# Kernel tuning notes

Measured on AMD Instinct MI355X. Metric: run time of the kernel, lower is better.

## Reference

```python
import jax, jax.numpy as jnp
import numpy as np

N_NODES = 50000
N_EDGES = 1600000
F_IN = 33
F_OUT = 128
HEADS = 2


def _add_self_loops(row, col, n):
    loop = jnp.arange(n, dtype=row.dtype)
    return jnp.concatenate([row, loop]), jnp.concatenate([col, loop])


def gcn_conv(x, row, col, w, W, b):
    # PyG GCNConv with edge_weight: add self-loops (weight 1), symmetric norm.
    n = x.shape[0]
    row, col = _add_self_loops(row, col, n)
    w = jnp.concatenate([w, jnp.ones((n,), x.dtype)])
    deg = jax.ops.segment_sum(w, col, num_segments=n)
    dinv = jnp.where(deg > 0, jax.lax.rsqrt(deg), 0.0)
    norm = dinv[row] * w * dinv[col]            # [E+N]
    xl = x @ W                                   # [N, F_OUT]
    out = jax.ops.segment_sum(norm[:, None] * xl[row], col, num_segments=n)
    return out + b


def gat_conv(x, row, col, W, att_src, att_dst, b):
    # PyG GATConv, heads=2, concat=False, eval-mode (no attention dropout).
    n = x.shape[0]
    row, col = _add_self_loops(row, col, n)
    xl = (x @ W).reshape(n, HEADS, F_OUT)        # [N, H, C]
    a_src = (xl * att_src).sum(-1)               # [N, H]
    a_dst = (xl * att_dst).sum(-1)               # [N, H]
    e = jax.nn.leaky_relu(a_src[row] + a_dst[col], 0.2)  # [E+N, H]
    m = jax.ops.segment_max(e, col, num_segments=n)      # per-dst max (stable)
    e = jnp.exp(e - m[col])
    s = jax.ops.segment_sum(e, col, num_segments=n)
    alpha = e / s[col]                           # edge softmax per dst node
    out = jax.ops.segment_sum(alpha[:, :, None] * xl[row], col, num_segments=n)
    return out.mean(axis=1) + b                  # concat=False -> head mean


def setup_inputs() -> dict:
    key = jax.random.key(0)
    ks = jax.random.split(key, 16)
    s_in = 1.0 / np.sqrt(F_IN)
    s_h = 1.0 / np.sqrt(F_OUT)
    inp = {
        "target_x": jax.random.normal(ks[0], (N_NODES, F_IN), jnp.float32),
        "target_edge_index": jax.random.randint(ks[1], (2, N_EDGES), 0, N_NODES, jnp.int32),
        "target_weight": jax.random.uniform(ks[2], (N_EDGES,), jnp.float32),
        "gcn_W": jax.random.normal(ks[3], (F_IN, F_OUT), jnp.float32) * s_in,
        "gcn_b": jnp.zeros((F_OUT,), jnp.float32),
        "gat1_W": jax.random.normal(ks[4], (F_OUT, HEADS * F_OUT), jnp.float32) * s_h,
        "gat1_as": jax.random.normal(ks[5], (HEADS, F_OUT), jnp.float32) * s_h,
        "gat1_ad": jax.random.normal(ks[6], (HEADS, F_OUT), jnp.float32) * s_h,
        "gat1_b": jnp.zeros((F_OUT,), jnp.float32),
        "gat2_W": jax.random.normal(ks[7], (F_OUT, HEADS * F_OUT), jnp.float32) * s_h,
        "gat2_as": jax.random.normal(ks[8], (HEADS, F_OUT), jnp.float32) * s_h,
        "gat2_ad": jax.random.normal(ks[9], (HEADS, F_OUT), jnp.float32) * s_h,
        "gat2_b": jnp.zeros((F_OUT,), jnp.float32),
        "fc1_W": jax.random.normal(ks[10], (F_OUT, F_OUT), jnp.float32) * s_h,
        "fc1_b": jnp.zeros((F_OUT,), jnp.float32),
        "fc2_W": jax.random.normal(ks[11], (F_OUT, F_OUT), jnp.float32) * s_h,
        "fc2_b": jnp.zeros((F_OUT,), jnp.float32),
        "pro_bias": jax.random.uniform(ks[12], (1, F_OUT), jnp.float32, -0.2, 0.2),
    }
    return inp


def _forward(target_x, target_weight, gcn_W, gcn_b, gat1_W, gat1_as, gat1_ad,
             gat1_b, gat2_W, gat2_as, gat2_ad, gat2_b, fc1_W, fc1_b,
             fc2_W, fc2_b, pro_bias, row, col):
    # layer 0: GCN + ReLU
    x = jax.nn.relu(gcn_conv(target_x, row, col, target_weight, gcn_W, gcn_b))
    # layer 1: GAT + ReLU, then sigmoid-gated blend
    xt = jax.nn.relu(gat_conv(x, row, col, gat1_W, gat1_as, gat1_ad, gat1_b))
    z = jax.nn.sigmoid(xt @ fc1_W + fc1_b + x @ fc2_W + fc2_b + pro_bias)
    x = z * xt + (1.0 - z) * x
    # layer 2: GAT (no ReLU on last layer), gated blend
    xt = gat_conv(x, row, col, gat2_W, gat2_as, gat2_ad, gat2_b)
    z = jax.nn.sigmoid(xt @ fc1_W + fc1_b + x @ fc2_W + fc2_b + pro_bias)
    return z * xt + (1.0 - z) * x


def reference(target_x, target_edge_index, target_weight, gcn_W, gcn_b,
              gat1_W, gat1_as, gat1_ad, gat1_b, gat2_W, gat2_as, gat2_ad,
              gat2_b, fc1_W, fc1_b, fc2_W, fc2_b, pro_bias):
    row, col = target_edge_index[0], target_edge_index[1]
    return _forward(target_x, target_weight, gcn_W, gcn_b, gat1_W, gat1_as,
                    gat1_ad, gat1_b, gat2_W, gat2_as, gat2_ad, gat2_b,
                    fc1_W, fc1_b, fc2_W, fc2_b, pro_bias, row, col)
```

## Files before the change

kernel.cpp:

```cpp
#include <hip/hip_runtime.h>

#define F_IN 33
#define FP 36
#define C 128
#define GROWS 16
#define MAXDEG 128

__device__ __forceinline__ unsigned short f2bf(float f) {
  unsigned u = __float_as_uint(f);
  unsigned r = (u + 0x7fff + ((u >> 16) & 1)) >> 16;
  return (unsigned short)r;
}
__device__ __forceinline__ unsigned pack2(float lo, float hi) {
  return (unsigned)f2bf(lo) | ((unsigned)f2bf(hi) << 16);
}
__device__ __forceinline__ float bflo(unsigned u) { return __uint_as_float(u << 16); }
__device__ __forceinline__ float bfhi(unsigned u) { return __uint_as_float(u & 0xffff0000u); }


__global__ void count_kernel(const int* __restrict__ col, const float* __restrict__ w,
                             int* __restrict__ cnt, float* __restrict__ deg, int E) {
  int e = blockIdx.x * blockDim.x + threadIdx.x;
  if (e < E) {
    int c = col[e];
    atomicAdd(&cnt[c], 1);
    atomicAdd(&deg[c], w[e]);
  }
}

__global__ void scan1_kernel(const int* __restrict__ cnt, int* __restrict__ out,
                             int* __restrict__ bsum, int n) {
  __shared__ int lds[256];
  int t = threadIdx.x;
  int base = blockIdx.x * 1024 + t * 4;
  int v0 = (base + 0 < n) ? cnt[base + 0] : 0;
  int v1 = (base + 1 < n) ? cnt[base + 1] : 0;
  int v2 = (base + 2 < n) ? cnt[base + 2] : 0;
  int v3 = (base + 3 < n) ? cnt[base + 3] : 0;
  int tot = v0 + v1 + v2 + v3;
  lds[t] = tot;
  __syncthreads();
  for (int o = 1; o < 256; o <<= 1) {
    int x = (t >= o) ? lds[t - o] : 0;
    __syncthreads();
    lds[t] += x;
    __syncthreads();
  }
  int excl = lds[t] - tot;
  if (t == 255) bsum[blockIdx.x] = lds[255];
  if (base + 0 < n) out[base + 0] = excl;
  if (base + 1 < n) out[base + 1] = excl + v0;
  if (base + 2 < n) out[base + 2] = excl + v0 + v1;
  if (base + 3 < n) out[base + 3] = excl + v0 + v1 + v2;
}

__global__ void scan2_kernel(int* __restrict__ bsum, int nb) {
  __shared__ int lds[256];
  int t = threadIdx.x;
  int v = (t < nb) ? bsum[t] : 0;
  lds[t] = v;
  __syncthreads();
  for (int o = 1; o < 256; o <<= 1) {
    int x = (t >= o) ? lds[t - o] : 0;
    __syncthreads();
    lds[t] += x;
    __syncthreads();
  }
  if (t < nb) bsum[t] = lds[t] - v;
}

__global__ void scan3_dinv_kernel(int* __restrict__ off, const int* __restrict__ bsum,
                                  const float* __restrict__ deg, float* __restrict__ dinv,
                                  int n, int N) {
  int i = blockIdx.x * blockDim.x + threadIdx.x;
  if (i < n) off[i] += bsum[i >> 10];
  if (i < N) dinv[i] = rsqrtf(deg[i] + 1.0f);
}

__global__ void scatter_kernel(const int* __restrict__ row, const int* __restrict__ col,
                               const float* __restrict__ w, const int* __restrict__ off,
                               const float* __restrict__ dinv, int* __restrict__ cur,
                               int2* __restrict__ sedge, int E) {
  int e = blockIdx.x * blockDim.x + threadIdx.x;
  if (e < E) {
    int c = col[e];
    int r = row[e];
    int p = off[c] + atomicAdd(&cur[c], 1);
    sedge[p] = make_int2(r, __float_as_int(dinv[r] * w[e]));
  }
}


__global__ void prep_dots_kernel(const float* __restrict__ W1, const float* __restrict__ as1,
                                 const float* __restrict__ ad1, const float* __restrict__ W2,
                                 const float* __restrict__ as2, const float* __restrict__ ad2,
                                 float* __restrict__ attv) {
  int t = blockIdx.x * 256 + threadIdx.x;
  if (t >= 1024) return;
  int layer = t >> 9, rem = t & 511, sd = rem >> 8, rem2 = rem & 255;
  int h = rem2 >> 7, k = rem2 & 127;
  const float* W = layer ? W2 : W1;
  const float* att = sd ? (layer ? ad2 : ad1) : (layer ? as2 : as1);
  float s = 0.f;
  for (int c2 = 0; c2 < C; c2++) s += W[k * 2 * C + h * C + c2] * att[h * C + c2];
  attv[t] = s;
}

__global__ void prep_repack_kernel(const float* __restrict__ W1, const float* __restrict__ W2,
                                   float* __restrict__ Wp1, float* __restrict__ Wp2) {
  int t = blockIdx.x * 256 + threadIdx.x;
  int layer = t >> 15, rem = t & 32767, hk = rem >> 7, j = rem & 127;
  int h = hk >> 7, k = hk & 127;
  const float* W = layer ? W2 : W1;
  float* Wp = layer ? Wp2 : Wp1;
  Wp[hk * C + j] = W[k * 2 * C + h * C + j];
}

__global__ void convert_x_kernel(const float* __restrict__ x, unsigned* __restrict__ X36U, int N) {
  int t = blockIdx.x * blockDim.x + threadIdx.x;
  if (t >= N * (FP / 2)) return;
  int n = t / (FP / 2);
  int p = t - n * (FP / 2);
  int c0 = 2 * p, c1 = 2 * p + 1;
  float f0 = (c0 < F_IN) ? x[n * F_IN + c0] : 0.f;
  float f1 = (c1 < F_IN) ? x[n * F_IN + c1] : 0.f;
  X36U[t] = pack2(f0, f1);
}


__global__ __launch_bounds__(256) void gcn_agg33_kernel(
    const unsigned* __restrict__ X36U, const int* __restrict__ off,
    const int2* __restrict__ sedge, const float* __restrict__ dinv,
    float* __restrict__ Xagg, int N) {
  int c = blockIdx.x * 4 + (threadIdx.x >> 6);
  if (c >= N) return;
  int l = threadIdx.x & 63;
  bool act = l < FP / 2;
  float dc = dinv[c];
  unsigned uc = act ? X36U[(unsigned)c * (FP / 2) + l] : 0u;
  float A0x = dc * bflo(uc), A0y = dc * bfhi(uc);
  float A1x = 0.f, A1y = 0.f, A2x = 0.f, A2y = 0.f, A3x = 0.f, A3y = 0.f;
  int p = off[c], p1 = off[c + 1];
  for (; p + 4 <= p1; p += 4) {
    int2 e0 = sedge[p + 0], e1 = sedge[p + 1], e2 = sedge[p + 2], e3 = sedge[p + 3];
    unsigned u0 = 0, u1 = 0, u2 = 0, u3 = 0;
    if (act) {
      u0 = X36U[(unsigned)e0.x * (FP / 2) + l];
      u1 = X36U[(unsigned)e1.x * (FP / 2) + l];
      u2 = X36U[(unsigned)e2.x * (FP / 2) + l];
      u3 = X36U[(unsigned)e3.x * (FP / 2) + l];
    }
    float w0 = __int_as_float(e0.y), w1 = __int_as_float(e1.y);
    float w2 = __int_as_float(e2.y), w3 = __int_as_float(e3.y);
    A0x += w0 * bflo(u0); A0y += w0 * bfhi(u0);
    A1x += w1 * bflo(u1); A1y += w1 * bfhi(u1);
    A2x += w2 * bflo(u2); A2y += w2 * bfhi(u2);
    A3x += w3 * bflo(u3); A3y += w3 * bfhi(u3);
  }
  for (; p < p1; p++) {
    int2 e0 = sedge[p];
    unsigned u0 = act ? X36U[(unsigned)e0.x * (FP / 2) + l] : 0u;
    float w0 = __int_as_float(e0.y);
    A0x += w0 * bflo(u0); A0y += w0 * bfhi(u0);
  }
  if (act) {
    float2 o;
    o.x = dc * (A0x + A1x + A2x + A3x);
    o.y = dc * (A0y + A1y + A2y + A3y);
    ((float2*)Xagg)[(unsigned)c * (FP / 2) + l] = o;
  }
}

__global__ void gemm36_kernel(const float* __restrict__ Xagg, const float* __restrict__ W,
                              const float* __restrict__ b, const float* __restrict__ ws,
                              const float* __restrict__ wd, float* __restrict__ H,
                              unsigned short* __restrict__ Hb, float* __restrict__ asrc,
                              float* __restrict__ adst, int N) {
  int n0 = blockIdx.x * GROWS;
  int j = threadIdx.x;
  __shared__ float xr[GROWS * FP];
  __shared__ float xls[GROWS * 132];
  {
    const float4* src = (const float4*)(Xagg + (size_t)n0 * FP);
    float4* dst = (float4*)xr;
    for (int i = j; i < GROWS * FP / 4; i += 128) dst[i] = src[i];
  }
  __syncthreads();
  float acc[GROWS];
  #pragma unroll
  for (int r = 0; r < GROWS; r++) acc[r] = 0.f;
  #pragma unroll 3
  for (int k = 0; k < F_IN; k++) {
    float wv = W[k * C + j];
    #pragma unroll
    for (int r = 0; r < GROWS; r++) acc[r] += xr[r * FP + k] * wv;
  }
  #pragma unroll
  for (int r = 0; r < GROWS; r++) {
    int n = n0 + r;
    float v = fmaxf(acc[r] + b[j], 0.f);
    if (n < N) {
      H[(size_t)n * C + j] = v;
      Hb[(size_t)n * C + j] = f2bf(v);
    }
    xls[r * 132 + j] = v;
  }
  __syncthreads();
  int r = j >> 3, sub = j & 7;
  float sa0 = 0.f, sd0 = 0.f, sa1 = 0.f, sd1 = 0.f;
  for (int k = sub; k < C; k += 8) {
    float v = xls[r * 132 + k];
    sa0 += v * ws[k];      sd0 += v * wd[k];
    sa1 += v * ws[C + k];  sd1 += v * wd[C + k];
  }
  #pragma unroll
  for (int o = 4; o > 0; o >>= 1) {
    sa0 += __shfl_down(sa0, o); sd0 += __shfl_down(sd0, o);
    sa1 += __shfl_down(sa1, o); sd1 += __shfl_down(sd1, o);
  }
  int n = n0 + r;
  if (sub == 0 && n < N) {
    asrc[n * 2 + 0] = sa0; adst[n * 2 + 0] = sd0;
    asrc[n * 2 + 1] = sa1; adst[n * 2 + 1] = sd1;
  }
}

__global__ __launch_bounds__(256) void gat_agg_kernel(
    const unsigned* __restrict__ HbU, const float* __restrict__ asrc,
    const float* __restrict__ adst, const int* __restrict__ off,
    const int2* __restrict__ sedge, unsigned* __restrict__ AggU, int N) {
  __shared__ float2 lsc[4][MAXDEG];
  int slot = threadIdx.x >> 6;
  int c = blockIdx.x * 4 + slot;
  if (c >= N) return;
  int l = threadIdx.x & 63;
  float2 adc = ((const float2*)adst)[c];
  float2 asc = ((const float2*)asrc)[c];
  int p0 = off[c], p1 = off[c + 1];
  int deg = p1 - p0;
  float e00 = asc.x + adc.x; e00 = e00 > 0.f ? e00 : 0.2f * e00;
  float e01 = asc.y + adc.y; e01 = e01 > 0.f ? e01 : 0.2f * e01;
  float m0 = e00, m1 = e01;
  for (int p = p0 + l; p < p1; p += 64) {
    int r = sedge[p].x;
    float2 av = ((const float2*)asrc)[r];
    float e0 = av.x + adc.x; e0 = e0 > 0.f ? e0 : 0.2f * e0;
    float e1 = av.y + adc.y; e1 = e1 > 0.f ? e1 : 0.2f * e1;
    int i = p - p0;
    if (i < MAXDEG) lsc[slot][i] = make_float2(e0, e1);
    m0 = fmaxf(m0, e0); m1 = fmaxf(m1, e1);
  }
  #pragma unroll
  for (int o = 32; o > 0; o >>= 1) {
    m0 = fmaxf(m0, __shfl_xor(m0, o));
    m1 = fmaxf(m1, __shfl_xor(m1, o));
  }
  int nl = deg < MAXDEG ? deg : MAXDEG;
  float s0 = 0.f, s1 = 0.f;
  for (int i = l; i < nl; i += 64) {
    float2 sc = lsc[slot][i];
    float a0 = __expf(sc.x - m0), a1 = __expf(sc.y - m1);
    lsc[slot][i] = make_float2(a0, a1);
    s0 += a0; s1 += a1;
  }
  for (int p = p0 + MAXDEG + l; p < p1; p += 64) {
    int r = sedge[p].x;
    float2 av = ((const float2*)asrc)[r];
    float e0 = av.x + adc.x; e0 = e0 > 0.f ? e0 : 0.2f * e0;
    float e1 = av.y + adc.y; e1 = e1 > 0.f ? e1 : 0.2f * e1;
    s0 += __expf(e0 - m0); s1 += __expf(e1 - m1);
  }
  #pragma unroll
  for (int o = 32; o > 0; o >>= 1) { s0 += __shfl_xor(s0, o); s1 += __shfl_xor(s1, o); }
  float w0 = __expf(e00 - m0), w1 = __expf(e01 - m1);
  s0 += w0; s1 += w1;
  float inv0 = 1.f / s0, inv1 = 1.f / s1;
  unsigned uc = HbU[(unsigned)c * 64 + l];
  float a00 = w0 * bflo(uc), a01 = w0 * bfhi(uc);
  float a10 = w1 * bflo(uc), a11 = w1 * bfhi(uc);
  float b00 = 0.f, b01 = 0.f, b10 = 0.f, b11 = 0.f;
  int i = 0;
  for (; i + 8 <= nl; i += 8) {
    int r0 = sedge[p0 + i + 0].x, r1 = sedge[p0 + i + 1].x;
    int r2 = sedge[p0 + i + 2].x, r3 = sedge[p0 + i + 3].x;
    int r4 = sedge[p0 + i + 4].x, r5 = sedge[p0 + i + 5].x;
    int r6 = sedge[p0 + i + 6].x, r7 = sedge[p0 + i + 7].x;
    unsigned u0 = HbU[(unsigned)r0 * 64 + l];
    unsigned u1 = HbU[(unsigned)r1 * 64 + l];
    unsigned u2 = HbU[(unsigned)r2 * 64 + l];
    unsigned u3 = HbU[(unsigned)r3 * 64 + l];
    unsigned u4 = HbU[(unsigned)r4 * 64 + l];
    unsigned u5 = HbU[(unsigned)r5 * 64 + l];
    unsigned u6 = HbU[(unsigned)r6 * 64 + l];
    unsigned u7 = HbU[(unsigned)r7 * 64 + l];
    float2 f0 = lsc[slot][i + 0], f1 = lsc[slot][i + 1];
    float2 f2 = lsc[slot][i + 2], f3 = lsc[slot][i + 3];
    float2 f4 = lsc[slot][i + 4], f5 = lsc[slot][i + 5];
    float2 f6 = lsc[slot][i + 6], f7 = lsc[slot][i + 7];
    a00 += f0.x * bflo(u0); a01 += f0.x * bfhi(u0); a10 += f0.y * bflo(u0); a11 += f0.y * bfhi(u0);
    b00 += f1.x * bflo(u1); b01 += f1.x * bfhi(u1); b10 += f1.y * bflo(u1); b11 += f1.y * bfhi(u1);
    a00 += f2.x * bflo(u2); a01 += f2.x * bfhi(u2); a10 += f2.y * bflo(u2); a11 += f2.y * bfhi(u2);
    b00 += f3.x * bflo(u3); b01 += f3.x * bfhi(u3); b10 += f3.y * bflo(u3); b11 += f3.y * bfhi(u3);
    a00 += f4.x * bflo(u4); a01 += f4.x * bfhi(u4); a10 += f4.y * bflo(u4); a11 += f4.y * bfhi(u4);
    b00 += f5.x * bflo(u5); b01 += f5.x * bfhi(u5); b10 += f5.y * bflo(u5); b11 += f5.y * bfhi(u5);
    a00 += f6.x * bflo(u6); a01 += f6.x * bfhi(u6); a10 += f6.y * bflo(u6); a11 += f6.y * bfhi(u6);
    b00 += f7.x * bflo(u7); b01 += f7.x * bfhi(u7); b10 += f7.y * bflo(u7); b11 += f7.y * bfhi(u7);
  }
  for (; i < nl; i++) {
    int r0 = sedge[p0 + i].x;
    unsigned u0 = HbU[(unsigned)r0 * 64 + l];
    float2 f0 = lsc[slot][i];
    a00 += f0.x * bflo(u0); a01 += f0.x * bfhi(u0);
    a10 += f0.y * bflo(u0); a11 += f0.y * bfhi(u0);
  }
  for (int p = p0 + MAXDEG; p < p1; p++) {
    int r = sedge[p].x;
    float2 av = ((const float2*)asrc)[r];
    float e0 = av.x + adc.x; e0 = e0 > 0.f ? e0 : 0.2f * e0;
    float e1 = av.y + adc.y; e1 = e1 > 0.f ? e1 : 0.2f * e1;
    float al0 = __expf(e0 - m0), al1 = __expf(e1 - m1);
    unsigned u0 = HbU[(unsigned)r * 64 + l];
    a00 += al0 * bflo(u0); a01 += al0 * bfhi(u0);
    a10 += al1 * bflo(u0); a11 += al1 * bfhi(u0);
  }
  AggU[(unsigned)c * 128 + l]      = pack2((a00 + b00) * inv0, (a01 + b01) * inv0);
  AggU[(unsigned)c * 128 + 64 + l] = pack2((a10 + b10) * inv1, (a11 + b11) * inv1);
}

__global__ void post_gemm_kernel(const unsigned* __restrict__ AggU, const float* __restrict__ Wp,
                                 const float* __restrict__ b, float* __restrict__ out,
                                 int relu, int N) {
  int n0 = blockIdx.x * GROWS;
  int j = threadIdx.x;
  __shared__ float als[GROWS * 260];
  {
    const uint2* src = (const uint2*)(AggU + (size_t)n0 * 128);
    for (int t = j; t < GROWS * 64; t += 128) {
      int row = t >> 6, cp = t & 63;
      uint2 u = (n0 + row < N) ? src[t] : make_uint2(0u, 0u);
      float* d = &als[row * 260 + cp * 4];
      d[0] = bflo(u.x); d[1] = bfhi(u.x); d[2] = bflo(u.y); d[3] = bfhi(u.y);
    }
  }
  __syncthreads();
  float acc[GROWS];
  #pragma unroll
  for (int r = 0; r < GROWS; r++) acc[r] = 0.f;
  #pragma unroll 2
  for (int k4 = 0; k4 < 256; k4 += 4) {
    float w0 = Wp[(k4 + 0) * C + j], w1 = Wp[(k4 + 1) * C + j];
    float w2 = Wp[(k4 + 2) * C + j], w3 = Wp[(k4 + 3) * C + j];
    #pragma unroll
    for (int r = 0; r < GROWS; r++) {
      float4 a = *(const float4*)&als[r * 260 + k4];
      acc[r] += a.x * w0 + a.y * w1 + a.z * w2 + a.w * w3;
    }
  }
  #pragma unroll
  for (int r = 0; r < GROWS; r++) {
    int n = n0 + r;
    if (n < N) {
      float v = 0.5f * acc[r] + b[j];
      if (relu) v = fmaxf(v, 0.f);
      out[(size_t)n * C + j] = v;
    }
  }
}

__global__ void blend_kernel(const float* __restrict__ xt, const float* __restrict__ x,
                             const float* __restrict__ fc1W, const float* __restrict__ fc1b,
                             const float* __restrict__ fc2W, const float* __restrict__ fc2b,
                             const float* __restrict__ pb, float* __restrict__ out,
                             unsigned short* __restrict__ Hb2, const float* __restrict__ ws,
                             const float* __restrict__ wd, float* __restrict__ asrc,
                             float* __restrict__ adst, int dots, int N) {
  int n0 = blockIdx.x * GROWS;
  int j = threadIdx.x;
  __shared__ float xtr[GROWS * C];
  __shared__ float xr[GROWS * C];
  __shared__ float xls[GROWS * 132];
  {
    float4* a4 = (float4*)xtr;
    float4* b4 = (float4*)xr;
    const float4* xt4 = (const float4*)xt;
    const float4* x4 = (const float4*)x;
    for (int i = j; i < GROWS * C / 4; i += 128) {
      int n = n0 + (i * 4) / C;
      if (n < N) {
        a4[i] = xt4[n0 * (C / 4) + i];
        b4[i] = x4[n0 * (C / 4) + i];
      } else {
        a4[i] = make_float4(0.f, 0.f, 0.f, 0.f);
        b4[i] = make_float4(0.f, 0.f, 0.f, 0.f);
      }
    }
  }
  __syncthreads();
  float s1[GROWS], s2[GROWS];
  #pragma unroll
  for (int r = 0; r < GROWS; r++) { s1[r] = 0.f; s2[r] = 0.f; }
  #pragma unroll 2
  for (int k4 = 0; k4 < C; k4 += 4) {
    float w1a = fc1W[(k4 + 0) * C + j], w2a = fc2W[(k4 + 0) * C + j];
    float w1b = fc1W[(k4 + 1) * C + j], w2b = fc2W[(k4 + 1) * C + j];
    float w1c = fc1W[(k4 + 2) * C + j], w2c = fc2W[(k4 + 2) * C + j];
    float w1d = fc1W[(k4 + 3) * C + j], w2d = fc2W[(k4 + 3) * C + j];
    #pragma unroll
    for (int r = 0; r < GROWS; r++) {
      float4 t4 = *(const float4*)&xtr[r * C + k4];
      float4 x4 = *(const float4*)&xr[r * C + k4];
      s1[r] += t4.x * w1a + t4.y * w1b + t4.z * w1c + t4.w * w1d;
      s2[r] += x4.x * w2a + x4.y * w2b + x4.z * w2c + x4.w * w2d;
    }
  }
  float bb = fc1b[j] + fc2b[j] + pb[j];
  #pragma unroll
  for (int r = 0; r < GROWS; r++) {
    int n = n0 + r;
    float t = s1[r] + s2[r] + bb;
    float z = 1.f / (1.f + __expf(-t));
    float o = z * xtr[r * C + j] + (1.f - z) * xr[r * C + j];
    if (n < N) {
      out[(size_t)n * C + j] = o;
      if (dots) Hb2[(size_t)n * C + j] = f2bf(o);
    }
    xls[r * 132 + j] = o;
  }
  if (!dots) return;
  __syncthreads();
  int r = j >> 3, sub = j & 7;
  float sa0 = 0.f, sd0 = 0.f, sa1 = 0.f, sd1 = 0.f;
  for (int k = sub; k < C; k += 8) {
    float v = xls[r * 132 + k];
    sa0 += v * ws[k];      sd0 += v * wd[k];
    sa1 += v * ws[C + k];  sd1 += v * wd[C + k];
  }
  #pragma unroll
  for (int o = 4; o > 0; o >>= 1) {
    sa0 += __shfl_down(sa0, o); sd0 += __shfl_down(sd0, o);
    sa1 += __shfl_down(sa1, o); sd1 += __shfl_down(sd1, o);
  }
  int n = n0 + r;
  if (sub == 0 && n < N) {
    asrc[n * 2 + 0] = sa0; adst[n * 2 + 0] = sd0;
    asrc[n * 2 + 1] = sa1; adst[n * 2 + 1] = sd1;
  }
}


extern "C" void kernel_launch(void* const* d_in, const int* in_sizes, int n_in,
                              void* d_out, int out_size, void* d_ws, size_t ws_size,
                              hipStream_t stream) {
  const float* x_in  = (const float*)d_in[0];
  const int*   ei    = (const int*)d_in[1];
  const float* ew    = (const float*)d_in[2];
  const float* gcn_W = (const float*)d_in[3];
  const float* gcn_b = (const float*)d_in[4];
  const float* g1_W  = (const float*)d_in[5];
  const float* g1_as = (const float*)d_in[6];
  const float* g1_ad = (const float*)d_in[7];
  const float* g1_b  = (const float*)d_in[8];
  const float* g2_W  = (const float*)d_in[9];
  const float* g2_as = (const float*)d_in[10];
  const float* g2_ad = (const float*)d_in[11];
  const float* g2_b  = (const float*)d_in[12];
  const float* fc1_W = (const float*)d_in[13];
  const float* fc1_b = (const float*)d_in[14];
  const float* fc2_W = (const float*)d_in[15];
  const float* fc2_b = (const float*)d_in[16];
  const float* pb    = (const float*)d_in[17];

  const int N = in_sizes[0] / F_IN;
  const int E = in_sizes[2];
  const int* row = ei;
  const int* col = ei + E;

  char* ws = (char*)d_ws;
  size_t o = 0;
  auto alloc = [&](size_t bytes) -> void* {
    void* p = ws + o;
    o += (bytes + 255) & ~(size_t)255;
    return p;
  };
  int*   cnt   = (int*)alloc((size_t)(N + 1) * 4);
  int*   cur   = (int*)alloc((size_t)N * 4);
  float* deg   = (float*)alloc((size_t)N * 4);
  size_t zero_bytes = o;
  int*   off   = (int*)alloc((size_t)(N + 1) * 4);
  float* dinv  = (float*)alloc((size_t)N * 4);
  int*   bsum  = (int*)alloc(256 * 4);
  int2*  sedge = (int2*)alloc((size_t)E * 8);
  float* attv  = (float*)alloc(1024 * 4);
  float* Wp1   = (float*)alloc((size_t)256 * C * 4);
  float* Wp2   = (float*)alloc((size_t)256 * C * 4);
  float* asrc  = (float*)alloc((size_t)N * 2 * 4);
  float* adst  = (float*)alloc((size_t)N * 2 * 4);
  unsigned* X36U = (unsigned*)alloc((size_t)N * (FP / 2) * 4);
  float* Xagg  = (float*)alloc((size_t)N * FP * 4);
  float* H     = (float*)alloc((size_t)N * C * 4);
  unsigned short* Hb  = (unsigned short*)alloc((size_t)N * C * 2);
  unsigned* AggU = (unsigned*)alloc((size_t)N * 128 * 4);
  float* XT    = (float*)alloc((size_t)N * C * 4);
  float* H2    = (float*)alloc((size_t)N * C * 4);
  unsigned short* Hb2 = (unsigned short*)alloc((size_t)N * C * 2);
  (void)ws_size; (void)n_in; (void)out_size;

  float* ws1 = attv + 0,   *wd1 = attv + 256;
  float* ws2 = attv + 512, *wd2 = attv + 768;

  hipMemsetAsync(d_ws, 0, zero_bytes, stream);

  const int tb = 256;
  const int nP = N + 1;
  const int nb = (nP + 1023) / 1024;

  prep_dots_kernel<<<4, 256, 0, stream>>>(g1_W, g1_as, g1_ad, g2_W, g2_as, g2_ad, attv);
  prep_repack_kernel<<<256, 256, 0, stream>>>(g1_W, g2_W, Wp1, Wp2);
  convert_x_kernel<<<(N * (FP / 2) + tb - 1) / tb, tb, 0, stream>>>(x_in, X36U, N);

  count_kernel<<<(E + tb - 1) / tb, tb, 0, stream>>>(col, ew, cnt, deg, E);
  scan1_kernel<<<nb, 256, 0, stream>>>(cnt, off, bsum, nP);
  scan2_kernel<<<1, 256, 0, stream>>>(bsum, nb);
  scan3_dinv_kernel<<<(nP + tb - 1) / tb, tb, 0, stream>>>(off, bsum, deg, dinv, nP, N);
  scatter_kernel<<<(E + tb - 1) / tb, tb, 0, stream>>>(row, col, ew, off, dinv, cur, sedge, E);

  gcn_agg33_kernel<<<(N + 3) / 4, 256, 0, stream>>>(X36U, off, sedge, dinv, Xagg, N);
  gemm36_kernel<<<(N + GROWS - 1) / GROWS, C, 0, stream>>>(Xagg, gcn_W, gcn_b, ws1, wd1,
                                                           H, Hb, asrc, adst, N);

  gat_agg_kernel<<<(N + 3) / 4, 256, 0, stream>>>((const unsigned*)Hb, asrc, adst, off, sedge, AggU, N);
  post_gemm_kernel<<<(N + GROWS - 1) / GROWS, C, 0, stream>>>(AggU, Wp1, g1_b, XT, 1, N);
  blend_kernel<<<(N + GROWS - 1) / GROWS, C, 0, stream>>>(XT, H, fc1_W, fc1_b, fc2_W, fc2_b, pb,
                                                          H2, Hb2, ws2, wd2, asrc, adst, 1, N);

  gat_agg_kernel<<<(N + 3) / 4, 256, 0, stream>>>((const unsigned*)Hb2, asrc, adst, off, sedge, AggU, N);
  post_gemm_kernel<<<(N + GROWS - 1) / GROWS, C, 0, stream>>>(AggU, Wp2, g2_b, XT, 0, N);
  blend_kernel<<<(N + GROWS - 1) / GROWS, C, 0, stream>>>(XT, H2, fc1_W, fc1_b, fc2_W, fc2_b, pb,
                                                          (float*)d_out, (unsigned short*)0,
                                                          ws2, wd2, asrc, adst, 0, N);
}
```

Measured before the change: 1.007 ms.

## Drop LDS staging in dense GEMM kernels and store GAT aggregates in fp32

The gemm36, post_gemm and blend kernels no longer copy their input rows into shared memory behind a barrier. Each thread now reads the row data directly from global memory as broadcast float4 loads, with a separate scalar path for the partial last tile. The GAT aggregation output changes from packed bf16 to fp32, so post_gemm skips the unpack step, at the cost of twice the intermediate memory traffic. Dropping LDS staging frees shared memory and may raise occupancy, but it relies on the cache to serve the repeated per-thread reads of the same addresses.

```diff
diff --git a/kernel.cpp b/kernel.cpp
--- a/kernel.cpp
+++ b/kernel.cpp
@@ -171,29 +171,37 @@
   }
 }
 
-__global__ void gemm36_kernel(const float* __restrict__ Xagg, const float* __restrict__ W,
-                              const float* __restrict__ b, const float* __restrict__ ws,
-                              const float* __restrict__ wd, float* __restrict__ H,
-                              unsigned short* __restrict__ Hb, float* __restrict__ asrc,
-                              float* __restrict__ adst, int N) {
+__global__ __launch_bounds__(128) void gemm36_kernel(
+    const float* __restrict__ Xagg, const float* __restrict__ W,
+    const float* __restrict__ b, const float* __restrict__ wsv,
+    const float* __restrict__ wdv, float* __restrict__ H,
+    unsigned short* __restrict__ Hb, float* __restrict__ asrc,
+    float* __restrict__ adst, int N) {
   int n0 = blockIdx.x * GROWS;
   int j = threadIdx.x;
-  __shared__ float xr[GROWS * FP];
   __shared__ float xls[GROWS * 132];
-  {
-    const float4* src = (const float4*)(Xagg + (size_t)n0 * FP);
-    float4* dst = (float4*)xr;
-    for (int i = j; i < GROWS * FP / 4; i += 128) dst[i] = src[i];
-  }
-  __syncthreads();
   float acc[GROWS];
   #pragma unroll
   for (int r = 0; r < GROWS; r++) acc[r] = 0.f;
-  #pragma unroll 3
-  for (int k = 0; k < F_IN; k++) {
-    float wv = W[k * C + j];
+  if (n0 + GROWS <= N) {
+    for (int k4 = 0; k4 < 32; k4 += 4) {
+      float w0 = W[(k4 + 0) * C + j], w1 = W[(k4 + 1) * C + j];
+      float w2 = W[(k4 + 2) * C + j], w3 = W[(k4 + 3) * C + j];
+      #pragma unroll
+      for (int r = 0; r < GROWS; r++) {
+        float4 a = *(const float4*)(Xagg + (size_t)(n0 + r) * FP + k4);
+        acc[r] += a.x * w0 + a.y * w1 + a.z * w2 + a.w * w3;
+      }
+    }
+    float w32 = W[32 * C + j];
     #pragma unroll
-    for (int r = 0; r < GROWS; r++) acc[r] += xr[r * FP + k] * wv;
+    for (int r = 0; r < GROWS; r++) acc[r] += Xagg[(size_t)(n0 + r) * FP + 32] * w32;
+  } else {
+    int nr = N - n0;
+    for (int k = 0; k < F_IN; k++) {
+      float wv = W[k * C + j];
+      for (int r = 0; r < nr; r++) acc[r] += Xagg[(size_t)(n0 + r) * FP + k] * wv;
+    }
   }
   #pragma unroll
   for (int r = 0; r < GROWS; r++) {
@@ -210,8 +218,8 @@
   float sa0 = 0.f, sd0 = 0.f, sa1 = 0.f, sd1 = 0.f;
   for (int k = sub; k < C; k += 8) {
     float v = xls[r * 132 + k];
-    sa0 += v * ws[k];      sd0 += v * wd[k];
-    sa1 += v * ws[C + k];  sd1 += v * wd[C + k];
+    sa0 += v * wsv[k];      sd0 += v * wdv[k];
+    sa1 += v * wsv[C + k];  sd1 += v * wdv[C + k];
   }
   #pragma unroll
   for (int o = 4; o > 0; o >>= 1) {
@@ -228,7 +236,7 @@
 __global__ __launch_bounds__(256) void gat_agg_kernel(
     const unsigned* __restrict__ HbU, const float* __restrict__ asrc,
     const float* __restrict__ adst, const int* __restrict__ off,
-    const int2* __restrict__ sedge, unsigned* __restrict__ AggU, int N) {
+    const int2* __restrict__ sedge, float* __restrict__ Agg, int N) {
   __shared__ float2 lsc[4][MAXDEG];
   int slot = threadIdx.x >> 6;
   int c = blockIdx.x * 4 + slot;
@@ -323,37 +331,33 @@
     a00 += al0 * bflo(u0); a01 += al0 * bfhi(u0);
     a10 += al1 * bflo(u0); a11 += al1 * bfhi(u0);
   }
-  AggU[(unsigned)c * 128 + l]      = pack2((a00 + b00) * inv0, (a01 + b01) * inv0);
-  AggU[(unsigned)c * 128 + 64 + l] = pack2((a10 + b10) * inv1, (a11 + b11) * inv1);
-}
-
-__global__ void post_gemm_kernel(const unsigned* __restrict__ AggU, const float* __restrict__ Wp,
-                                 const float* __restrict__ b, float* __restrict__ out,
-                                 int relu, int N) {
+  ((float2*)Agg)[(size_t)c * 128 + l]      = make_float2((a00 + b00) * inv0, (a01 + b01) * inv0);
+  ((float2*)Agg)[(size_t)c * 128 + 64 + l] = make_float2((a10 + b10) * inv1, (a11 + b11) * inv1);
+}
+
+__global__ __launch_bounds__(128) void post_gemm_kernel(
+    const float* __restrict__ Agg, const float* __restrict__ Wp,
+    const float* __restrict__ b, float* __restrict__ out, int relu, int N) {
   int n0 = blockIdx.x * GROWS;
   int j = threadIdx.x;
-  __shared__ float als[GROWS * 260];
-  {
-    const uint2* src = (const uint2*)(AggU + (size_t)n0 * 128);
-    for (int t = j; t < GROWS * 64; t += 128) {
-      int row = t >> 6, cp = t & 63;
-      uint2 u = (n0 + row < N) ? src[t] : make_uint2(0u, 0u);
-      float* d = &als[row * 260 + cp * 4];
-      d[0] = bflo(u.x); d[1] = bfhi(u.x); d[2] = bflo(u.y); d[3] = bfhi(u.y);
-    }
-  }
-  __syncthreads();
   float acc[GROWS];
   #pragma unroll
   for (int r = 0; r < GROWS; r++) acc[r] = 0.f;
-  #pragma unroll 2
-  for (int k4 = 0; k4 < 256; k4 += 4) {
-    float w0 = Wp[(k4 + 0) * C + j], w1 = Wp[(k4 + 1) * C + j];
-    float w2 = Wp[(k4 + 2) * C + j], w3 = Wp[(k4 + 3) * C + j];
-    #pragma unroll
-    for (int r = 0; r < GROWS; r++) {
-      float4 a = *(const float4*)&als[r * 260 + k4];
-      acc[r] += a.x * w0 + a.y * w1 + a.z * w2 + a.w * w3;
+  if (n0 + GROWS <= N) {
+    for (int k4 = 0; k4 < 256; k4 += 4) {
+      float w0 = Wp[(k4 + 0) * C + j], w1 = Wp[(k4 + 1) * C + j];
+      float w2 = Wp[(k4 + 2) * C + j], w3 = Wp[(k4 + 3) * C + j];
+      #pragma unroll
+      for (int r = 0; r < GROWS; r++) {
+        float4 a = *(const float4*)(Agg + (size_t)(n0 + r) * 256 + k4);
+        acc[r] += a.x * w0 + a.y * w1 + a.z * w2 + a.w * w3;
+      }
+    }
+  } else {
+    int nr = N - n0;
+    for (int k = 0; k < 256; k++) {
+      float wv = Wp[k * C + j];
+      for (int r = 0; r < nr; r++) acc[r] += Agg[(size_t)(n0 + r) * 256 + k] * wv;
     }
   }
   #pragma unroll
@@ -367,64 +371,60 @@
   }
 }
 
-__global__ void blend_kernel(const float* __restrict__ xt, const float* __restrict__ x,
-                             const float* __restrict__ fc1W, const float* __restrict__ fc1b,
-                             const float* __restrict__ fc2W, const float* __restrict__ fc2b,
-                             const float* __restrict__ pb, float* __restrict__ out,
-                             unsigned short* __restrict__ Hb2, const float* __restrict__ ws,
-                             const float* __restrict__ wd, float* __restrict__ asrc,
-                             float* __restrict__ adst, int dots, int N) {
+__global__ __launch_bounds__(128) void blend_kernel(
+    const float* __restrict__ xt, const float* __restrict__ x,
+    const float* __restrict__ fc1W, const float* __restrict__ fc1b,
+    const float* __restrict__ fc2W, const float* __restrict__ fc2b,
+    const float* __restrict__ pb, float* __restrict__ out,
+    unsigned short* __restrict__ Hb2, const float* __restrict__ wsv,
+    const float* __restrict__ wdv, float* __restrict__ asrc,
+    float* __restrict__ adst, int dots, int N) {
   int n0 = blockIdx.x * GROWS;
   int j = threadIdx.x;
-  __shared__ float xtr[GROWS * C];
-  __shared__ float xr[GROWS * C];
   __shared__ float xls[GROWS * 132];
-  {
-    float4* a4 = (float4*)xtr;
-    float4* b4 = (float4*)xr;
-    const float4* xt4 = (const float4*)xt;
-    const float4* x4 = (const float4*)x;
-    for (int i = j; i < GROWS * C / 4; i += 128) {
-      int n = n0 + (i * 4) / C;
-      if (n < N) {
-        a4[i] = xt4[n0 * (C / 4) + i];
-        b4[i] = x4[n0 * (C / 4) + i];
-      } else {
-        a4[i] = make_float4(0.f, 0.f, 0.f, 0.f);
-        b4[i] = make_float4(0.f, 0.f, 0.f, 0.f);
+  float s1[GROWS], s2[GROWS];
+  #pragma unroll
+  for (int r = 0; r < GROWS; r++) { s1[r] = 0.f; s2[r] = 0.f; }
+  if (n0 + GROWS <= N) {
+    for (int k4 = 0; k4 < C; k4 += 4) {
+      float w1a = fc1W[(k4 + 0) * C + j], w2a = fc2W[(k4 + 0) * C + j];
+      float w1b = fc1W[(k4 + 1) * C + j], w2b = fc2W[(k4 + 1) * C + j];
+      float w1c = fc1W[(k4 + 2) * C + j], w2c = fc2W[(k4 + 2) * C + j];
+      float w1d = fc1W[(k4 + 3) * C + j], w2d = fc2W[(k4 + 3) * C + j];
+      #pragma unroll
+      for (int r = 0; r < GROWS; r++) {
+        float4 t4 = *(const float4*)(xt + (size_t)(n0 + r) * C + k4);
+        float4 x4 = *(const float4*)(x + (size_t)(n0 + r) * C + k4);
+        s1[r] += t4.x * w1a + t4.y * w1b + t4.z * w1c + t4.w * w1d;
+        s2[r] += x4.x * w2a + x4.y * w2b + x4.z * w2c + x4.w * w2d;
       }
     }
-  }
-  __syncthreads();
-  float s1[GROWS], s2[GROWS];
-  #pragma unroll
-  for (int r = 0; r < GROWS; r++) { s1[r] = 0.f; s2[r] = 0.f; }
-  #pragma unroll 2
-  for (int k4 = 0; k4 < C; k4 += 4) {
-    float w1a = fc1W[(k4 + 0) * C + j], w2a = fc2W[(k4 + 0) * C + j];
-    float w1b = fc1W[(k4 + 1) * C + j], w2b = fc2W[(k4 + 1) * C + j];
-    float w1c = fc1W[(k4 + 2) * C + j], w2c = fc2W[(k4 + 2) * C + j];
-    float w1d = fc1W[(k4 + 3) * C + j], w2d = fc2W[(k4 + 3) * C + j];
-    #pragma unroll
-    for (int r = 0; r < GROWS; r++) {
-      float4 t4 = *(const float4*)&xtr[r * C + k4];
-      float4 x4 = *(const float4*)&xr[r * C + k4];
-      s1[r] += t4.x * w1a + t4.y * w1b + t4.z * w1c + t4.w * w1d;
-      s2[r] += x4.x * w2a + x4.y * w2b + x4.z * w2c + x4.w * w2d;
+  } else {
+    int nr = N - n0;
+    for (int k = 0; k < C; k++) {
+      float w1 = fc1W[k * C + j], w2 = fc2W[k * C + j];
+      for (int r = 0; r < nr; r++) {
+        s1[r] += xt[(size_t)(n0 + r) * C + k] * w1;
+        s2[r] += x[(size_t)(n0 + r) * C + k] * w2;
+      }
     }
   }
   float bb = fc1b[j] + fc2b[j] + pb[j];
   #pragma unroll
   for (int r = 0; r < GROWS; r++) {
     int n = n0 + r;
-    float t = s1[r] + s2[r] + bb;
-    float z = 1.f / (1.f + __expf(-t));
-    float o = z * xtr[r * C + j] + (1.f - z) * xr[r * C + j];
     if (n < N) {
+      float xtv = xt[(size_t)n * C + j];
+      float xv  = x[(size_t)n * C + j];
+      float t = s1[r] + s2[r] + bb;
+      float z = 1.f / (1.f + __expf(-t));
+      float o = z * xtv + (1.f - z) * xv;
       out[(size_t)n * C + j] = o;
       if (dots) Hb2[(size_t)n * C + j] = f2bf(o);
-    }
-    xls[r * 132 + j] = o;
+      xls[r * 132 + j] = o;
+    } else {
+      xls[r * 132 + j] = 0.f;
+    }
   }
   if (!dots) return;
   __syncthreads();
@@ -432,8 +432,8 @@
   float sa0 = 0.f, sd0 = 0.f, sa1 = 0.f, sd1 = 0.f;
   for (int k = sub; k < C; k += 8) {
     float v = xls[r * 132 + k];
-    sa0 += v * ws[k];      sd0 += v * wd[k];
-    sa1 += v * ws[C + k];  sd1 += v * wd[C + k];
+    sa0 += v * wsv[k];      sd0 += v * wdv[k];
+    sa1 += v * wsv[C + k];  sd1 += v * wdv[C + k];
   }
   #pragma unroll
   for (int o = 4; o > 0; o >>= 1) {
@@ -499,7 +499,7 @@
   float* Xagg  = (float*)alloc((size_t)N * FP * 4);
   float* H     = (float*)alloc((size_t)N * C * 4);
   unsigned short* Hb  = (unsigned short*)alloc((size_t)N * C * 2);
-  unsigned* AggU = (unsigned*)alloc((size_t)N * 128 * 4);
+  float* Agg   = (float*)alloc((size_t)N * 256 * 4);
   float* XT    = (float*)alloc((size_t)N * C * 4);
   float* H2    = (float*)alloc((size_t)N * C * 4);
   unsigned short* Hb2 = (unsigned short*)alloc((size_t)N * C * 2);
@@ -528,13 +528,13 @@
   gemm36_kernel<<<(N + GROWS - 1) / GROWS, C, 0, stream>>>(Xagg, gcn_W, gcn_b, ws1, wd1,
                                                            H, Hb, asrc, adst, N);
 
-  gat_agg_kernel<<<(N + 3) / 4, 256, 0, stream>>>((const unsigned*)Hb, asrc, adst, off, sedge, AggU, N);
-  post_gemm_kernel<<<(N + GROWS - 1) / GROWS, C, 0, stream>>>(AggU, Wp1, g1_b, XT, 1, N);
+  gat_agg_kernel<<<(N + 3) / 4, 256, 0, stream>>>((const unsigned*)Hb, asrc, adst, off, sedge, Agg, N);
+  post_gemm_kernel<<<(N + GROWS - 1) / GROWS, C, 0, stream>>>(Agg, Wp1, g1_b, XT, 1, N);
   blend_kernel<<<(N + GROWS - 1) / GROWS, C, 0, stream>>>(XT, H, fc1_W, fc1_b, fc2_W, fc2_b, pb,
                                                           H2, Hb2, ws2, wd2, asrc, adst, 1, N);
 
-  gat_agg_kernel<<<(N + 3) / 4, 256, 0, stream>>>((const unsigned*)Hb2, asrc, adst, off, sedge, AggU, N);
-  post_gemm_kernel<<<(N + GROWS - 1) / GROWS, C, 0, stream>>>(AggU, Wp2, g2_b, XT, 0, N);
+  gat_agg_kernel<<<(N + 3) / 4, 256, 0, stream>>>((const unsigned*)Hb2, asrc, adst, off, sedge, Agg, N);
+  post_gemm_kernel<<<(N + GROWS - 1) / GROWS, C, 0, stream>>>(Agg, Wp2, g2_b, XT, 0, N);
   blend_kernel<<<(N + GROWS - 1) / GROWS, C, 0, stream>>>(XT, H2, fc1_W, fc1_b, fc2_W, fc2_b, pb,
                                                           (float*)d_out, (unsigned short*)0,
                                                           ws2, wd2, asrc, adst, 0, N);
```

Result: slower. 1.299 ms (+29.0%).

## Restructure post-GEMM and blend GEMMs with bf16 LDS tiles and 2x8 register blocking

Applied to the files above, without the earlier changes.

The post-GEMM and blend kernels now keep the row tile in shared memory as packed bf16 and read it with uint4 loads. Each thread computes two output columns for eight rows, so every weight load is reused across more multiply-adds. The blend GEMM merges fc1 and fc2 into one K=256 product over a concatenated weight matrix Wz, reading bf16 copies of xt and x, which post_gemm now also writes as XTb. The aim is less LDS traffic and fewer global weight loads per FMA, at the cost of one extra bf16 output buffer and bf16 rounding of the gate inputs.

```diff
diff --git a/kernel.cpp b/kernel.cpp
--- a/kernel.cpp
+++ b/kernel.cpp
@@ -114,6 +114,13 @@
   const float* W = layer ? W2 : W1;
   float* Wp = layer ? Wp2 : Wp1;
   Wp[hk * C + j] = W[k * 2 * C + h * C + j];
+}
+
+__global__ void prep_wz_kernel(const float* __restrict__ fc1W, const float* __restrict__ fc2W,
+                               float* __restrict__ Wz) {
+  int t = blockIdx.x * 256 + threadIdx.x;
+  if (t >= 32768) return;
+  Wz[t] = (t < 16384) ? fc1W[t] : fc2W[t - 16384];
 }
 
 __global__ void convert_x_kernel(const float* __restrict__ x, unsigned* __restrict__ X36U, int N) {
@@ -172,8 +179,8 @@
 }
 
 __global__ void gemm36_kernel(const float* __restrict__ Xagg, const float* __restrict__ W,
-                              const float* __restrict__ b, const float* __restrict__ ws,
-                              const float* __restrict__ wd, float* __restrict__ H,
+                              const float* __restrict__ b, const float* __restrict__ wsv,
+                              const float* __restrict__ wdv, float* __restrict__ H,
                               unsigned short* __restrict__ Hb, float* __restrict__ asrc,
                               float* __restrict__ adst, int N) {
   int n0 = blockIdx.x * GROWS;
@@ -210,8 +217,8 @@
   float sa0 = 0.f, sd0 = 0.f, sa1 = 0.f, sd1 = 0.f;
   for (int k = sub; k < C; k += 8) {
     float v = xls[r * 132 + k];
-    sa0 += v * ws[k];      sd0 += v * wd[k];
-    sa1 += v * ws[C + k];  sd1 += v * wd[C + k];
+    sa0 += v * wsv[k];      sd0 += v * wdv[k];
+    sa1 += v * wsv[C + k];  sd1 += v * wdv[C + k];
   }
   #pragma unroll
   for (int o = 4; o > 0; o >>= 1) {
@@ -327,113 +334,145 @@
   AggU[(unsigned)c * 128 + 64 + l] = pack2((a10 + b10) * inv1, (a11 + b11) * inv1);
 }
 
-__global__ void post_gemm_kernel(const unsigned* __restrict__ AggU, const float* __restrict__ Wp,
-                                 const float* __restrict__ b, float* __restrict__ out,
-                                 int relu, int N) {
+__global__ __launch_bounds__(128) void post_gemm_kernel(
+    const unsigned* __restrict__ AggU, const float* __restrict__ Wp,
+    const float* __restrict__ b, float* __restrict__ XT,
+    unsigned short* __restrict__ XTb, int relu, int N) {
+  __shared__ unsigned az[GROWS][128];
   int n0 = blockIdx.x * GROWS;
-  int j = threadIdx.x;
-  __shared__ float als[GROWS * 260];
+  int t = threadIdx.x;
   {
-    const uint2* src = (const uint2*)(AggU + (size_t)n0 * 128);
-    for (int t = j; t < GROWS * 64; t += 128) {
-      int row = t >> 6, cp = t & 63;
-      uint2 u = (n0 + row < N) ? src[t] : make_uint2(0u, 0u);
-      float* d = &als[row * 260 + cp * 4];
-      d[0] = bflo(u.x); d[1] = bfhi(u.x); d[2] = bflo(u.y); d[3] = bfhi(u.y);
-    }
-  }
-  __syncthreads();
-  float acc[GROWS];
-  #pragma unroll
-  for (int r = 0; r < GROWS; r++) acc[r] = 0.f;
-  #pragma unroll 2
-  for (int k4 = 0; k4 < 256; k4 += 4) {
-    float w0 = Wp[(k4 + 0) * C + j], w1 = Wp[(k4 + 1) * C + j];
-    float w2 = Wp[(k4 + 2) * C + j], w3 = Wp[(k4 + 3) * C + j];
+    const uint4* src = (const uint4*)AggU;
+    for (int i = t; i < GROWS * 32; i += 128) {
+      int r = i >> 5, cch = i & 31;
+      int n = n0 + r;
+      uint4 v = (n < N) ? src[(size_t)n * 32 + cch] : make_uint4(0u, 0u, 0u, 0u);
+      *(uint4*)&az[r][cch * 4] = v;
+    }
+  }
+  __syncthreads();
+  int w = t >> 6;
+  int l = t & 63;
+  float acc0[8], acc1[8];
+  #pragma unroll
+  for (int r = 0; r < 8; r++) { acc0[r] = 0.f; acc1[r] = 0.f; }
+  for (int k8 = 0; k8 < 256; k8 += 8) {
+    float wA[8], wB[8];
     #pragma unroll
-    for (int r = 0; r < GROWS; r++) {
-      float4 a = *(const float4*)&als[r * 260 + k4];
-      acc[r] += a.x * w0 + a.y * w1 + a.z * w2 + a.w * w3;
-    }
-  }
-  #pragma unroll
-  for (int r = 0; r < GROWS; r++) {
-    int n = n0 + r;
+    for (int q = 0; q < 8; q++) {
+      wA[q] = Wp[(k8 + q) * C + l];
+      wB[q] = Wp[(k8 + q) * C + l + 64];
+    }
+    #pragma unroll
+    for (int r = 0; r < 8; r++) {
+      uint4 u = *(const uint4*)&az[w * 8 + r][k8 >> 1];
+      float v0 = bflo(u.x), v1 = bfhi(u.x), v2 = bflo(u.y), v3 = bfhi(u.y);
+      float v4 = bflo(u.z), v5 = bfhi(u.z), v6 = bflo(u.w), v7 = bfhi(u.w);
+      acc0[r] += v0*wA[0] + v1*wA[1] + v2*wA[2] + v3*wA[3]
+               + v4*wA[4] + v5*wA[5] + v6*wA[6] + v7*wA[7];
+      acc1[r] += v0*wB[0] + v1*wB[1] + v2*wB[2] + v3*wB[3]
+               + v4*wB[4] + v5*wB[5] + v6*wB[6] + v7*wB[7];
+    }
+  }
+  float bA = b[l], bB = b[l + 64];
+  #pragma unroll
+  for (int r = 0; r < 8; r++) {
+    int n = n0 + w * 8 + r;
     if (n < N) {
-      float v = 0.5f * acc[r] + b[j];
-      if (relu) v = fmaxf(v, 0.f);
-      out[(size_t)n * C + j] = v;
-    }
-  }
-}
-
-__global__ void blend_kernel(const float* __restrict__ xt, const float* __restrict__ x,
-                             const float* __restrict__ fc1W, const float* __restrict__ fc1b,
-                             const float* __restrict__ fc2W, const float* __restrict__ fc2b,
-                             const float* __restrict__ pb, float* __restrict__ out,
-                             unsigned short* __restrict__ Hb2, const float* __restrict__ ws,
-                             const float* __restrict__ wd, float* __restrict__ asrc,
-                             float* __restrict__ adst, int dots, int N) {
+      float vA = 0.5f * acc0[r] + bA;
+      float vB = 0.5f * acc1[r] + bB;
+      if (relu) { vA = fmaxf(vA, 0.f); vB = fmaxf(vB, 0.f); }
+      XT[(size_t)n * C + l]      = vA;
+      XT[(size_t)n * C + l + 64] = vB;
+      XTb[(size_t)n * C + l]      = f2bf(vA);
+      XTb[(size_t)n * C + l + 64] = f2bf(vB);
+    }
+  }
+}
+
+__global__ __launch_bounds__(128) void blend_kernel(
+    const unsigned* __restrict__ XTbU, const unsigned* __restrict__ XbU,
+    const float* __restrict__ XTf, const float* __restrict__ Xf,
+    const float* __restrict__ Wz, const float* __restrict__ fc1b,
+    const float* __restrict__ fc2b, const float* __restrict__ pb,
+    float* __restrict__ out, unsigned short* __restrict__ Hb2,
+    const float* __restrict__ wsv, const float* __restrict__ wdv,
+    float* __restrict__ asrc, float* __restrict__ adst, int dots, int N) {
+  __shared__ unsigned az[GROWS][128];
+  __shared__ float xls[GROWS * 132];
   int n0 = blockIdx.x * GROWS;
-  int j = threadIdx.x;
-  __shared__ float xtr[GROWS * C];
-  __shared__ float xr[GROWS * C];
-  __shared__ float xls[GROWS * 132];
+  int t = threadIdx.x;
   {
-    float4* a4 = (float4*)xtr;
-    float4* b4 = (float4*)xr;
-    const float4* xt4 = (const float4*)xt;
-    const float4* x4 = (const float4*)x;
-    for (int i = j; i < GROWS * C / 4; i += 128) {
-      int n = n0 + (i * 4) / C;
-      if (n < N) {
-        a4[i] = xt4[n0 * (C / 4) + i];
-        b4[i] = x4[n0 * (C / 4) + i];
-      } else {
-        a4[i] = make_float4(0.f, 0.f, 0.f, 0.f);
-        b4[i] = make_float4(0.f, 0.f, 0.f, 0.f);
+    const uint4* s1 = (const uint4*)XTbU;
+    const uint4* s2 = (const uint4*)XbU;
+    for (int i = t; i < GROWS * 32; i += 128) {
+      int r = i >> 5, cch = i & 31;
+      int n = n0 + r;
+      uint4 v;
+      if (n < N) v = (cch < 16) ? s1[(size_t)n * 16 + cch] : s2[(size_t)n * 16 + (cch - 16)];
+      else v = make_uint4(0u, 0u, 0u, 0u);
+      *(uint4*)&az[r][cch * 4] = v;
+    }
+  }
+  __syncthreads();
+  int w = t >> 6;
+  int l = t & 63;
+  float acc0[8], acc1[8];
+  #pragma unroll
+  for (int r = 0; r < 8; r++) { acc0[r] = 0.f; acc1[r] = 0.f; }
+  for (int k8 = 0; k8 < 256; k8 += 8) {
+    float wA[8], wB[8];
+    #pragma unroll
+    for (int q = 0; q < 8; q++) {
+      wA[q] = Wz[(k8 + q) * C + l];
+      wB[q] = Wz[(k8 + q) * C + l + 64];
+    }
+    #pragma unroll
+    for (int r = 0; r < 8; r++) {
+      uint4 u = *(const uint4*)&az[w * 8 + r][k8 >> 1];
+      float v0 = bflo(u.x), v1 = bfhi(u.x), v2 = bflo(u.y), v3 = bfhi(u.y);
+      float v4 = bflo(u.z), v5 = bfhi(u.z), v6 = bflo(u.w), v7 = bfhi(u.w);
+      acc0[r] += v0*wA[0] + v1*wA[1] + v2*wA[2] + v3*wA[3]
+               + v4*wA[4] + v5*wA[5] + v6*wA[6] + v7*wA[7];
+      acc1[r] += v0*wB[0] + v1*wB[1] + v2*wB[2] + v3*wB[3]
+               + v4*wB[4] + v5*wB[5] + v6*wB[6] + v7*wB[7];
+    }
+  }
+  float bbA = fc1b[l] + fc2b[l] + pb[l];
+  float bbB = fc1b[l + 64] + fc2b[l + 64] + pb[l + 64];
+  #pragma unroll
+  for (int r = 0; r < 8; r++) {
+    int rr = w * 8 + r;
+    int n = n0 + rr;
+    if (n < N) {
+      float xtA = XTf[(size_t)n * C + l],      xA = Xf[(size_t)n * C + l];
+      float xtB = XTf[(size_t)n * C + l + 64], xB = Xf[(size_t)n * C + l + 64];
+      float tA = acc0[r] + bbA, tB = acc1[r] + bbB;
+      float zA = 1.f / (1.f + __expf(-tA));
+      float zB = 1.f / (1.f + __expf(-tB));
+      float oA = zA * xtA + (1.f - zA) * xA;
+      float oB = zB * xtB + (1.f - zB) * xB;
+      out[(size_t)n * C + l]      = oA;
+      out[(size_t)n * C + l + 64] = oB;
+      if (dots) {
+        Hb2[(size_t)n * C + l]      = f2bf(oA);
+        Hb2[(size_t)n * C + l + 64] = f2bf(oB);
       }
-    }
-  }
-  __syncthreads();
-  float s1[GROWS], s2[GROWS];
-  #pragma unroll
-  for (int r = 0; r < GROWS; r++) { s1[r] = 0.f; s2[r] = 0.f; }
-  #pragma unroll 2
-  for (int k4 = 0; k4 < C; k4 += 4) {
-    float w1a = fc1W[(k4 + 0) * C + j], w2a = fc2W[(k4 + 0) * C + j];
-    float w1b = fc1W[(k4 + 1) * C + j], w2b = fc2W[(k4 + 1) * C + j];
-    float w1c = fc1W[(k4 + 2) * C + j], w2c = fc2W[(k4 + 2) * C + j];
-    float w1d = fc1W[(k4 + 3) * C + j], w2d = fc2W[(k4 + 3) * C + j];
-    #pragma unroll
-    for (int r = 0; r < GROWS; r++) {
-      float4 t4 = *(const float4*)&xtr[r * C + k4];
-      float4 x4 = *(const float4*)&xr[r * C + k4];
-      s1[r] += t4.x * w1a + t4.y * w1b + t4.z * w1c + t4.w * w1d;
-      s2[r] += x4.x * w2a + x4.y * w2b + x4.z * w2c + x4.w * w2d;
-    }
-  }
-  float bb = fc1b[j] + fc2b[j] + pb[j];
-  #pragma unroll
-  for (int r = 0; r < GROWS; r++) {
-    int n = n0 + r;
-    float t = s1[r] + s2[r] + bb;
-    float z = 1.f / (1.f + __expf(-t));
-    float o = z * xtr[r * C + j] + (1.f - z) * xr[r * C + j];
-    if (n < N) {
-      out[(size_t)n * C + j] = o;
-      if (dots) Hb2[(size_t)n * C + j] = f2bf(o);
-    }
-    xls[r * 132 + j] = o;
+      xls[rr * 132 + l] = oA;
+      xls[rr * 132 + l + 64] = oB;
+    } else {
+      xls[rr * 132 + l] = 0.f;
+      xls[rr * 132 + l + 64] = 0.f;
+    }
   }
   if (!dots) return;
   __syncthreads();
-  int r = j >> 3, sub = j & 7;
+  int r = t >> 3, sub = t & 7;
   float sa0 = 0.f, sd0 = 0.f, sa1 = 0.f, sd1 = 0.f;
   for (int k = sub; k < C; k += 8) {
     float v = xls[r * 132 + k];
-    sa0 += v * ws[k];      sd0 += v * wd[k];
-    sa1 += v * ws[C + k];  sd1 += v * wd[C + k];
+    sa0 += v * wsv[k];      sd0 += v * wdv[k];
+    sa1 += v * wsv[C + k];  sd1 += v * wdv[C + k];
   }
   #pragma unroll
   for (int o = 4; o > 0; o >>= 1) {
@@ -493,6 +532,7 @@
   float* attv  = (float*)alloc(1024 * 4);
   float* Wp1   = (float*)alloc((size_t)256 * C * 4);
   float* Wp2   = (float*)alloc((size_t)256 * C * 4);
+  float* Wz    = (float*)alloc((size_t)256 * C * 4);
   float* asrc  = (float*)alloc((size_t)N * 2 * 4);
   float* adst  = (float*)alloc((size_t)N * 2 * 4);
   unsigned* X36U = (unsigned*)alloc((size_t)N * (FP / 2) * 4);
@@ -501,6 +541,7 @@
   unsigned short* Hb  = (unsigned short*)alloc((size_t)N * C * 2);
   unsigned* AggU = (unsigned*)alloc((size_t)N * 128 * 4);
   float* XT    = (float*)alloc((size_t)N * C * 4);
+  unsigned short* XTb = (unsigned short*)alloc((size_t)N * C * 2);
   float* H2    = (float*)alloc((size_t)N * C * 4);
   unsigned short* Hb2 = (unsigned short*)alloc((size_t)N * C * 2);
   (void)ws_size; (void)n_in; (void)out_size;
@@ -516,6 +557,7 @@
 
   prep_dots_kernel<<<4, 256, 0, stream>>>(g1_W, g1_as, g1_ad, g2_W, g2_as, g2_ad, attv);
   prep_repack_kernel<<<256, 256, 0, stream>>>(g1_W, g2_W, Wp1, Wp2);
+  prep_wz_kernel<<<128, 256, 0, stream>>>(fc1_W, fc2_W, Wz);
   convert_x_kernel<<<(N * (FP / 2) + tb - 1) / tb, tb, 0, stream>>>(x_in, X36U, N);
 
   count_kernel<<<(E + tb - 1) / tb, tb, 0, stream>>>(col, ew, cnt, deg, E);
@@ -529,13 +571,14 @@
                                                            H, Hb, asrc, adst, N);
 
   gat_agg_kernel<<<(N + 3) / 4, 256, 0, stream>>>((const unsigned*)Hb, asrc, adst, off, sedge, AggU, N);
-  post_gemm_kernel<<<(N + GROWS - 1) / GROWS, C, 0, stream>>>(AggU, Wp1, g1_b, XT, 1, N);
-  blend_kernel<<<(N + GROWS - 1) / GROWS, C, 0, stream>>>(XT, H, fc1_W, fc1_b, fc2_W, fc2_b, pb,
-                                                          H2, Hb2, ws2, wd2, asrc, adst, 1, N);
+  post_gemm_kernel<<<(N + GROWS - 1) / GROWS, C, 0, stream>>>(AggU, Wp1, g1_b, XT, XTb, 1, N);
+  blend_kernel<<<(N + GROWS - 1) / GROWS, C, 0, stream>>>(
+      (const unsigned*)XTb, (const unsigned*)Hb, XT, H, Wz, fc1_b, fc2_b, pb,
+      H2, Hb2, ws2, wd2, asrc, adst, 1, N);
 
   gat_agg_kernel<<<(N + 3) / 4, 256, 0, stream>>>((const unsigned*)Hb2, asrc, adst, off, sedge, AggU, N);
-  post_gemm_kernel<<<(N + GROWS - 1) / GROWS, C, 0, stream>>>(AggU, Wp2, g2_b, XT, 0, N);
-  blend_kernel<<<(N + GROWS - 1) / GROWS, C, 0, stream>>>(XT, H2, fc1_W, fc1_b, fc2_W, fc2_b, pb,
-                                                          (float*)d_out, (unsigned short*)0,
-                                                          ws2, wd2, asrc, adst, 0, N);
-}
+  post_gemm_kernel<<<(N + GROWS - 1) / GROWS, C, 0, stream>>>(AggU, Wp2, g2_b, XT, XTb, 0, N);
+  blend_kernel<<<(N + GROWS - 1) / GROWS, C, 0, stream>>>(
+      (const unsigned*)XTb, (const unsigned*)Hb2, XT, H2, Wz, fc1_b, fc2_b, pb,
+      (float*)d_out, (unsigned short*)0, ws2, wd2, asrc, adst, 0, N);
+}
```

Result: no change. 1.009 ms (+0.2%).
